# Performance work log

Measured on AMD Instinct MI355X. Metric: run time of the kernel, lower is better.

The kernel has to match this reference:

```python
import jax, jax.numpy as jnp
import numpy as np

N_FFT = 2048
HOP = 512
WIN = 2048
PAD = N_FFT // 2  # center padding, n_fft // 2


def setup_inputs() -> dict:
    key = jax.random.key(0)
    x = jax.random.normal(key, (16, 262144), dtype=jnp.float32)
    # periodic Hann window, identical to torch.hann_window(2048)
    window = (0.5 - 0.5 * jnp.cos(2.0 * jnp.pi * jnp.arange(WIN) / WIN)).astype(jnp.float32)
    return {"x": x, "window": window}


def reference(x, window):
    # x: [B, T]; center reflect-pad by n_fft//2 on both sides (matches F.pad mode='reflect')
    xp = jnp.pad(x, ((0, 0), (PAD, PAD)), mode="reflect")
    n_frames = (xp.shape[-1] - N_FFT) // HOP + 1  # static
    # strided framing (replaces the identity-conv im2col in the original)
    idx = jnp.arange(n_frames)[:, None] * HOP + jnp.arange(N_FFT)[None, :]  # [F, n_fft]
    frames = xp[:, idx] * window  # [B, F, n_fft], windowed frames
    # windowed DFT; rfft of windowed frame == F.linear(frames, fft_k) in the original
    spec = jnp.fft.rfft(frames, axis=-1)  # [B, F, n_fft//2+1] complex
    real = jnp.real(spec).transpose(0, 2, 1)  # [B, dim, F]
    imag = jnp.imag(spec).transpose(0, 2, 1)  # [B, dim, F]
    return (real, imag)
```

## Files before the change

### kernel.cpp

```cpp
#include <hip/hip_runtime.h>


#define N_FFT   2048
#define LOG2N   11
#define HOP     512
#define PADL    1024
#define NBINS   1025
#define NFRAMES 513
#define NBATCH  16
#define TLEN    262144

#define HALF_OUT ((size_t)NBATCH * NBINS * NFRAMES)

__device__ __forceinline__ int pidx(int a) { return a + (a >> 5); }

__device__ __forceinline__ int refl(int j) {
    if (j < 0)          j = -j;
    else if (j >= TLEN) j = 2 * TLEN - 2 - j;
    return j;
}

__device__ __forceinline__ int brev11(int n) {
    return (int)(__brev((unsigned)n) >> 21);
}

__device__ __forceinline__ float2 cmul(float2 a, float2 w) {
    return make_float2(fmaf(a.x, w.x, -a.y * w.y), fmaf(a.x, w.y, a.y * w.x));
}
__device__ __forceinline__ float2 cadd(float2 a, float2 b) {
    return make_float2(a.x + b.x, a.y + b.y);
}
__device__ __forceinline__ float2 csub(float2 a, float2 b) {
    return make_float2(a.x - b.x, a.y - b.y);
}
__device__ __forceinline__ float2 csqr(float2 w) {
    return make_float2(fmaf(w.x, w.x, -w.y * w.y), 2.0f * w.x * w.y);
}

template <int H, int L2H>
__device__ __forceinline__ void octet_pass(float2* __restrict__ zc, int q) {
    const int p    = q & (H - 1);
    const int base = ((q >> L2H) << (L2H + 3)) + p;
    int ia[8];
#pragma unroll
    for (int m = 0; m < 8; ++m) ia[m] = pidx(base + m * H);
    float2 v0 = zc[ia[0]], v1 = zc[ia[1]], v2 = zc[ia[2]], v3 = zc[ia[3]];
    float2 v4 = zc[ia[4]], v5 = zc[ia[5]], v6 = zc[ia[6]], v7 = zc[ia[7]];

    float2 w1, w2, w3;
    if (H == 1) {
        w3 = make_float2(1.0f, 0.0f); w2 = w3; w1 = w3;
    } else {
        float s, c;
        __sincosf((float)p * (-3.14159265358979323846f / (4.0f * (float)H)), &s, &c);
        w3 = make_float2(c, s);
        w2 = csqr(w3);
        w1 = csqr(w2);
    }

    float2 t;
    t = cmul(v1, w1); v1 = csub(v0, t); v0 = cadd(v0, t);
    t = cmul(v3, w1); v3 = csub(v2, t); v2 = cadd(v2, t);
    t = cmul(v5, w1); v5 = csub(v4, t); v4 = cadd(v4, t);
    t = cmul(v7, w1); v7 = csub(v6, t); v6 = cadd(v6, t);
    const float2 w2m = make_float2(w2.y, -w2.x);
    t = cmul(v2, w2);  v2 = csub(v0, t); v0 = cadd(v0, t);
    t = cmul(v3, w2m); v3 = csub(v1, t); v1 = cadd(v1, t);
    t = cmul(v6, w2);  v6 = csub(v4, t); v4 = cadd(v4, t);
    t = cmul(v7, w2m); v7 = csub(v5, t); v5 = cadd(v5, t);
    const float R = 0.70710678118654752f;
    const float2 w3o  = make_float2((w3.x + w3.y) * R, (w3.y - w3.x) * R);
    const float2 w3m  = make_float2(w3.y, -w3.x);
    const float2 w3mo = make_float2(w3o.y, -w3o.x);
    t = cmul(v4, w3);   v4 = csub(v0, t); v0 = cadd(v0, t);
    t = cmul(v5, w3o);  v5 = csub(v1, t); v1 = cadd(v1, t);
    t = cmul(v6, w3m);  v6 = csub(v2, t); v2 = cadd(v2, t);
    t = cmul(v7, w3mo); v7 = csub(v3, t); v3 = cadd(v3, t);

    zc[ia[0]] = v0; zc[ia[1]] = v1; zc[ia[2]] = v2; zc[ia[3]] = v3;
    zc[ia[4]] = v4; zc[ia[5]] = v5; zc[ia[6]] = v6; zc[ia[7]] = v7;
}

__device__ __forceinline__ void quad_core(float2* __restrict__ zc, int p,
                                          float2 w1, float2 w2, float2 w2m) {
    const int i0 = pidx(p), i1 = pidx(p + 512), i2 = pidx(p + 1024), i3 = pidx(p + 1536);
    float2 v0 = zc[i0], v1 = zc[i1], v2 = zc[i2], v3 = zc[i3];
    float2 t;
    t = cmul(v1, w1); v1 = csub(v0, t); v0 = cadd(v0, t);
    t = cmul(v3, w1); v3 = csub(v2, t); v2 = cadd(v2, t);
    t = cmul(v2, w2);  v2 = csub(v0, t); v0 = cadd(v0, t);
    t = cmul(v3, w2m); v3 = csub(v1, t); v1 = cadd(v1, t);
    zc[i0] = v0; zc[i1] = v1; zc[i2] = v2; zc[i3] = v3;
}

__global__ __launch_bounds__(512, 8) void stft_one(
    const float* __restrict__ x,
    const float* __restrict__ window,
    float* __restrict__ out)
{
    __shared__ float2 z[2][2113];

    const int d   = blockIdx.x;
    const int tid = threadIdx.x;
    float* __restrict__ outr = out;
    float* __restrict__ outi = out + HALF_OUT;

    if (d < NBATCH) {
        const int b = d;
        const float* xb = x + (size_t)b * TLEN;
        const int a0 = 512 * HOP - PADL;
#pragma unroll
        for (int it = 0; it < 4; ++it) {
            const int n = tid + it * 512;
            const float w  = window[n];
            const float va = xb[refl(a0 + n)] * w;
            const float vb = xb[refl(a0 + HOP + n)] * w;
            z[0][pidx(brev11(n))] = make_float2(va, vb);
        }
        __syncthreads();
        if (tid < 256) octet_pass<1, 0>(z[0], tid);
        __syncthreads();
        if (tid < 256) octet_pass<8, 3>(z[0], tid);
        __syncthreads();
        if (tid < 256) octet_pass<64, 6>(z[0], tid);
        __syncthreads();
        {
            float s, cc;
            __sincosf((float)tid * (-3.14159265358979323846f / 1024.0f), &s, &cc);
            const float2 w2  = make_float2(cc, s);
            const float2 w1  = csqr(w2);
            const float2 w2m = make_float2(w2.y, -w2.x);
            quad_core(z[0], tid, w1, w2, w2m);
        }
        __syncthreads();
#pragma unroll
        for (int it = 0; it < 3; ++it) {
            const int k = tid + it * 512;
            if (k < NBINS) {
                const int km = (N_FFT - k) & (N_FFT - 1);
                const float2 zk = z[0][pidx(k)];
                const float2 zr = z[0][pidx(km)];
                const size_t o = ((size_t)b * NBINS + (size_t)k) * NFRAMES + 512;
                outr[o] = 0.5f * (zk.x + zr.x);
                outi[o] = 0.5f * (zk.y - zr.y);
            }
        }
        return;
    }

    const int m    = d - NBATCH;
    const int xcd  = m & 7;
    const int slot = m >> 3;
    const int O    = (slot >> 3) * 8 + xcd;
    const int L    = O * 8 + (slot & 7);
    const int b    = L >> 7;
    const int g    = L & 127;
    const int f0   = g * 4;

    const float* xb = x + (size_t)b * TLEN;

    if (g >= 1 && g <= 126) {
#pragma unroll
        for (int it = 0; it < 2; ++it) {
            const int idx = tid + it * 512;
            const int c   = idx >> 9;
            const int j   = idx & 511;
            const int n0  = j << 2;
            const int a0  = (f0 + 2 * c) * HOP - PADL;
            const float4 w4 = *reinterpret_cast<const float4*>(&window[n0]);
            const float4 a4 = *reinterpret_cast<const float4*>(&xb[a0 + n0]);
            const float4 b4 = *reinterpret_cast<const float4*>(&xb[a0 + HOP + n0]);
            const int r0 = (int)(__brev((unsigned)j) >> 23);
            z[c][pidx(r0)]        = make_float2(a4.x * w4.x, b4.x * w4.x);
            z[c][pidx(r0 + 1024)] = make_float2(a4.y * w4.y, b4.y * w4.y);
            z[c][pidx(r0 + 512)]  = make_float2(a4.z * w4.z, b4.z * w4.z);
            z[c][pidx(r0 + 1536)] = make_float2(a4.w * w4.w, b4.w * w4.w);
        }
    } else {
#pragma unroll
        for (int it = 0; it < 8; ++it) {
            const int idx = tid + it * 512;
            const int c   = idx >> 11;
            const int n   = idx & 2047;
            const int fa  = f0 + 2 * c;
            const float w  = window[n];
            const float va = xb[refl(fa * HOP - PADL + n)] * w;
            const float vb = xb[refl((fa + 1) * HOP - PADL + n)] * w;
            z[c][pidx(brev11(n))] = make_float2(va, vb);
        }
    }
    __syncthreads();

    {
        const int c = tid >> 8, q = tid & 255;
        octet_pass<1, 0>(z[c], q);  __syncthreads();
        octet_pass<8, 3>(z[c], q);  __syncthreads();
        octet_pass<64, 6>(z[c], q); __syncthreads();
    }

    {
        const int p = tid;
        float s, cc;
        __sincosf((float)p * (-3.14159265358979323846f / 1024.0f), &s, &cc);
        const float2 w2  = make_float2(cc, s);
        const float2 w1  = csqr(w2);
        const float2 w2m = make_float2(w2.y, -w2.x);
        quad_core(z[0], p, w1, w2, w2m);
        quad_core(z[1], p, w1, w2, w2m);
    }
    __syncthreads();

#pragma unroll
    for (int it = 0; it < 3; ++it) {
        const int k = tid + it * 512;
        if (k < NBINS) {
            const int km = (N_FFT - k) & (N_FFT - 1);
            const float2 zk0 = z[0][pidx(k)];
            const float2 zr0 = z[0][pidx(km)];
            const float2 zk1 = z[1][pidx(k)];
            const float2 zr1 = z[1][pidx(km)];
            const size_t o = ((size_t)b * NBINS + (size_t)k) * NFRAMES + (size_t)f0;
            outr[o + 0] = 0.5f * (zk0.x + zr0.x);
            outr[o + 1] = 0.5f * (zk0.y + zr0.y);
            outr[o + 2] = 0.5f * (zk1.x + zr1.x);
            outr[o + 3] = 0.5f * (zk1.y + zr1.y);
            outi[o + 0] = 0.5f * (zk0.y - zr0.y);
            outi[o + 1] = 0.5f * (zr0.x - zk0.x);
            outi[o + 2] = 0.5f * (zk1.y - zr1.y);
            outi[o + 3] = 0.5f * (zr1.x - zk1.x);
        }
    }
}

extern "C" void kernel_launch(void* const* d_in, const int* in_sizes, int n_in,
                              void* d_out, int out_size, void* d_ws, size_t ws_size,
                              hipStream_t stream) {
    const float* x      = (const float*)d_in[0];
    const float* window = (const float*)d_in[1];
    float* out          = (float*)d_out;

    dim3 grid(2064);
    stft_one<<<grid, 512, 0, stream>>>(x, window, out);
}
```

Baseline: 104.2 us.

## Split work to one frame-pair FFT per 256-thread block with register-held final stage

Each block now computes one packed complex FFT (two real frames) with 256 threads instead of two FFTs with 512 threads, doubling the grid and halving shared memory per block. The last radix-4 stage keeps its outputs in registers and writes only the mirrored half back to LDS, so the postprocess reads fewer LDS values. Output stores become 2-wide float vector stores per bin row, and the XCD-aware block remap is adjusted for the new grid. The aim is more resident blocks, fewer LDS round trips, and fewer store instructions. The cost is narrower 8-byte output writes instead of four adjacent scalars, plus a 4-byte-aligned vector type whose store width depends on what the compiler emits.

```diff
diff --git a/kernel.cpp b/kernel.cpp
--- a/kernel.cpp
+++ b/kernel.cpp
@@ -11,6 +11,9 @@
 #define TLEN    262144
 
 #define HALF_OUT ((size_t)NBATCH * NBINS * NFRAMES)
+
+typedef float f2_t __attribute__((ext_vector_type(2)));
+typedef f2_t uf2 __attribute__((aligned(4)));
 
 __device__ __forceinline__ int pidx(int a) { return a + (a >> 5); }
 
@@ -93,12 +96,24 @@
     zc[i0] = v0; zc[i1] = v1; zc[i2] = v2; zc[i3] = v3;
 }
 
-__global__ __launch_bounds__(512, 8) void stft_one(
+__device__ __forceinline__ void store_row2(float* __restrict__ pr,
+                                           float* __restrict__ pi,
+                                           float2 zk, float2 zr) {
+    uf2 re, im;
+    re.x = 0.5f * (zk.x + zr.x);
+    re.y = 0.5f * (zk.y + zr.y);
+    im.x = 0.5f * (zk.y - zr.y);
+    im.y = 0.5f * (zr.x - zk.x);
+    *reinterpret_cast<uf2*>(pr) = re;
+    *reinterpret_cast<uf2*>(pi) = im;
+}
+
+__global__ __launch_bounds__(256, 8) void stft_one(
     const float* __restrict__ x,
     const float* __restrict__ window,
     float* __restrict__ out)
 {
-    __shared__ float2 z[2][2113];
+    __shared__ float2 z[2113];
 
     const int d   = blockIdx.x;
     const int tid = threadIdx.x;
@@ -110,40 +125,35 @@
         const float* xb = x + (size_t)b * TLEN;
         const int a0 = 512 * HOP - PADL;
 #pragma unroll
-        for (int it = 0; it < 4; ++it) {
-            const int n = tid + it * 512;
+        for (int it = 0; it < 8; ++it) {
+            const int n = tid + it * 256;
             const float w  = window[n];
             const float va = xb[refl(a0 + n)] * w;
             const float vb = xb[refl(a0 + HOP + n)] * w;
-            z[0][pidx(brev11(n))] = make_float2(va, vb);
+            z[pidx(brev11(n))] = make_float2(va, vb);
         }
         __syncthreads();
-        if (tid < 256) octet_pass<1, 0>(z[0], tid);
-        __syncthreads();
-        if (tid < 256) octet_pass<8, 3>(z[0], tid);
-        __syncthreads();
-        if (tid < 256) octet_pass<64, 6>(z[0], tid);
-        __syncthreads();
-        {
+        octet_pass<1, 0>(z, tid);  __syncthreads();
+        octet_pass<8, 3>(z, tid);  __syncthreads();
+        octet_pass<64, 6>(z, tid); __syncthreads();
+#pragma unroll
+        for (int it = 0; it < 2; ++it) {
+            const int p = tid + it * 256;
             float s, cc;
-            __sincosf((float)tid * (-3.14159265358979323846f / 1024.0f), &s, &cc);
+            __sincosf((float)p * (-3.14159265358979323846f / 1024.0f), &s, &cc);
             const float2 w2  = make_float2(cc, s);
             const float2 w1  = csqr(w2);
             const float2 w2m = make_float2(w2.y, -w2.x);
-            quad_core(z[0], tid, w1, w2, w2m);
+            quad_core(z, p, w1, w2, w2m);
         }
         __syncthreads();
-#pragma unroll
-        for (int it = 0; it < 3; ++it) {
-            const int k = tid + it * 512;
-            if (k < NBINS) {
-                const int km = (N_FFT - k) & (N_FFT - 1);
-                const float2 zk = z[0][pidx(k)];
-                const float2 zr = z[0][pidx(km)];
-                const size_t o = ((size_t)b * NBINS + (size_t)k) * NFRAMES + 512;
-                outr[o] = 0.5f * (zk.x + zr.x);
-                outi[o] = 0.5f * (zk.y - zr.y);
-            }
+        for (int k = tid; k < NBINS; k += 256) {
+            const int km = (N_FFT - k) & (N_FFT - 1);
+            const float2 zk = z[pidx(k)];
+            const float2 zr = z[pidx(km)];
+            const size_t o = ((size_t)b * NBINS + (size_t)k) * NFRAMES + 512;
+            outr[o] = 0.5f * (zk.x + zr.x);
+            outi[o] = 0.5f * (zk.y - zr.y);
         }
         return;
     }
@@ -151,84 +161,78 @@
     const int m    = d - NBATCH;
     const int xcd  = m & 7;
     const int slot = m >> 3;
-    const int O    = (slot >> 3) * 8 + xcd;
-    const int L    = O * 8 + (slot & 7);
-    const int b    = L >> 7;
-    const int g    = L & 127;
-    const int f0   = g * 4;
+    const int G    = (slot >> 4) * 8 + xcd;
+    const int L    = G * 16 + (slot & 15);
+    const int b    = L >> 8;
+    const int g    = L & 255;
+    const int f0   = g * 2;
 
     const float* xb = x + (size_t)b * TLEN;
-
-    if (g >= 1 && g <= 126) {
+    const int a0    = f0 * HOP - PADL;
+
+    if (g >= 1 && g <= 254) {
 #pragma unroll
         for (int it = 0; it < 2; ++it) {
-            const int idx = tid + it * 512;
-            const int c   = idx >> 9;
-            const int j   = idx & 511;
-            const int n0  = j << 2;
-            const int a0  = (f0 + 2 * c) * HOP - PADL;
+            const int j  = tid + it * 256;
+            const int n0 = j << 2;
             const float4 w4 = *reinterpret_cast<const float4*>(&window[n0]);
             const float4 a4 = *reinterpret_cast<const float4*>(&xb[a0 + n0]);
             const float4 b4 = *reinterpret_cast<const float4*>(&xb[a0 + HOP + n0]);
             const int r0 = (int)(__brev((unsigned)j) >> 23);
-            z[c][pidx(r0)]        = make_float2(a4.x * w4.x, b4.x * w4.x);
-            z[c][pidx(r0 + 1024)] = make_float2(a4.y * w4.y, b4.y * w4.y);
-            z[c][pidx(r0 + 512)]  = make_float2(a4.z * w4.z, b4.z * w4.z);
-            z[c][pidx(r0 + 1536)] = make_float2(a4.w * w4.w, b4.w * w4.w);
+            z[pidx(r0)]        = make_float2(a4.x * w4.x, b4.x * w4.x);
+            z[pidx(r0 + 1024)] = make_float2(a4.y * w4.y, b4.y * w4.y);
+            z[pidx(r0 + 512)]  = make_float2(a4.z * w4.z, b4.z * w4.z);
+            z[pidx(r0 + 1536)] = make_float2(a4.w * w4.w, b4.w * w4.w);
         }
     } else {
 #pragma unroll
         for (int it = 0; it < 8; ++it) {
-            const int idx = tid + it * 512;
-            const int c   = idx >> 11;
-            const int n   = idx & 2047;
-            const int fa  = f0 + 2 * c;
+            const int n = tid + it * 256;
             const float w  = window[n];
-            const float va = xb[refl(fa * HOP - PADL + n)] * w;
-            const float vb = xb[refl((fa + 1) * HOP - PADL + n)] * w;
-            z[c][pidx(brev11(n))] = make_float2(va, vb);
+            const float va = xb[refl(a0 + n)] * w;
+            const float vb = xb[refl(a0 + HOP + n)] * w;
+            z[pidx(brev11(n))] = make_float2(va, vb);
         }
     }
     __syncthreads();
 
-    {
-        const int c = tid >> 8, q = tid & 255;
-        octet_pass<1, 0>(z[c], q);  __syncthreads();
-        octet_pass<8, 3>(z[c], q);  __syncthreads();
-        octet_pass<64, 6>(z[c], q); __syncthreads();
-    }
-
-    {
-        const int p = tid;
+    octet_pass<1, 0>(z, tid);  __syncthreads();
+    octet_pass<8, 3>(z, tid);  __syncthreads();
+    octet_pass<64, 6>(z, tid); __syncthreads();
+
+    float2 V0[2], V1[2], V2[2];
+#pragma unroll
+    for (int itq = 0; itq < 2; ++itq) {
+        const int p = tid + itq * 256;
         float s, cc;
         __sincosf((float)p * (-3.14159265358979323846f / 1024.0f), &s, &cc);
         const float2 w2  = make_float2(cc, s);
         const float2 w1  = csqr(w2);
         const float2 w2m = make_float2(w2.y, -w2.x);
-        quad_core(z[0], p, w1, w2, w2m);
-        quad_core(z[1], p, w1, w2, w2m);
+        float2 v0 = z[pidx(p)];
+        float2 v1 = z[pidx(p + 512)];
+        float2 v2 = z[pidx(p + 1024)];
+        float2 v3 = z[pidx(p + 1536)];
+        float2 t;
+        t = cmul(v1, w1); v1 = csub(v0, t); v0 = cadd(v0, t);
+        t = cmul(v3, w1); v3 = csub(v2, t); v2 = cadd(v2, t);
+        t = cmul(v2, w2);  v2 = csub(v0, t); v0 = cadd(v0, t);
+        t = cmul(v3, w2m); v3 = csub(v1, t); v1 = cadd(v1, t);
+        z[pidx(p + 1024)] = v2;
+        z[pidx(p + 1536)] = v3;
+        V0[itq] = v0; V1[itq] = v1; V2[itq] = v2;
     }
     __syncthreads();
 
-#pragma unroll
-    for (int it = 0; it < 3; ++it) {
-        const int k = tid + it * 512;
-        if (k < NBINS) {
-            const int km = (N_FFT - k) & (N_FFT - 1);
-            const float2 zk0 = z[0][pidx(k)];
-            const float2 zr0 = z[0][pidx(km)];
-            const float2 zk1 = z[1][pidx(k)];
-            const float2 zr1 = z[1][pidx(km)];
-            const size_t o = ((size_t)b * NBINS + (size_t)k) * NFRAMES + (size_t)f0;
-            outr[o + 0] = 0.5f * (zk0.x + zr0.x);
-            outr[o + 1] = 0.5f * (zk0.y + zr0.y);
-            outr[o + 2] = 0.5f * (zk1.x + zr1.x);
-            outr[o + 3] = 0.5f * (zk1.y + zr1.y);
-            outi[o + 0] = 0.5f * (zk0.y - zr0.y);
-            outi[o + 1] = 0.5f * (zr0.x - zk0.x);
-            outi[o + 2] = 0.5f * (zk1.y - zr1.y);
-            outi[o + 3] = 0.5f * (zr1.x - zk1.x);
-        }
+    const size_t rbase = ((size_t)b * NBINS + (size_t)tid) * NFRAMES + (size_t)f0;
+    const size_t rowS  = (size_t)256 * NFRAMES;
+    const float2 zr1 = (tid == 0) ? V0[0] : z[pidx(2048 - tid)];
+    store_row2(outr + rbase, outi + rbase, V0[0], zr1);
+    store_row2(outr + rbase + rowS, outi + rbase + rowS, V0[1], z[pidx(1792 - tid)]);
+    store_row2(outr + rbase + 2 * rowS, outi + rbase + 2 * rowS, V1[0], z[pidx(1536 - tid)]);
+    store_row2(outr + rbase + 3 * rowS, outi + rbase + 3 * rowS, V1[1], z[pidx(1280 - tid)]);
+    if (tid == 0) {
+        store_row2(outr + rbase + 4 * rowS, outi + rbase + 4 * rowS, V2[0], V2[0]);
     }
 }
 
@@ -239,6 +243,6 @@
     const float* window = (const float*)d_in[1];
     float* out          = (float*)d_out;
 
-    dim3 grid(2064);
-    stft_one<<<grid, 512, 0, stream>>>(x, window, out);
-}
+    dim3 grid(4112);
+    stft_one<<<grid, 256, 0, stream>>>(x, window, out);
+}
```

New measurement: 119.8 us. 15.0% more time.
